# Optimization experiments

Hardware: AMD Instinct MI355X
Metric: run time of the kernel (lower is better)

Reference implementation:

```python
import jax, jax.numpy as jnp
import numpy as np

B, IH, IW = 16, 32, 32
N = IH * IW
HEADS, DIM_HEAD = 8, 64
INNER = HEADS * DIM_HEAD  # 512
INP, OUP = 512, 512
SCALE = DIM_HEAD ** -0.5


def _relative_index():
    # replicate torch.meshgrid (ij) -> coords [2, N]
    yy, xx = np.meshgrid(np.arange(IH), np.arange(IW), indexing='ij')
    coords = np.stack([yy.reshape(-1), xx.reshape(-1)])  # [2, N]
    rel = coords[:, :, None] - coords[:, None, :]        # [2, N, N]
    rel[0] += IH - 1
    rel[1] += IW - 1
    rel[0] *= 2 * IW - 1
    return jnp.asarray(rel.sum(0).reshape(-1), dtype=jnp.int32)  # [N*N]


def setup_inputs() -> dict:
    key = jax.random.key(0)
    k1, k2, k3, k4, k5 = jax.random.split(key, 5)
    x = jax.random.normal(k1, (B, N, INP), dtype=jnp.float32)
    W_qkv = jax.random.normal(k2, (INP, 3 * INNER), dtype=jnp.float32) * (INP ** -0.5)
    # table is initialized to zeros in the module; use small randn so bias path is exercised
    rel_table = jax.random.normal(k3, ((2 * IH - 1) * (2 * IW - 1), HEADS), dtype=jnp.float32) * 0.02
    W_out = jax.random.normal(k4, (INNER, OUP), dtype=jnp.float32) * (INNER ** -0.5)
    b_out = jax.random.normal(k5, (OUP,), dtype=jnp.float32) * 0.02
    return {
        'x': x,
        'W_qkv': W_qkv,
        'rel_table': rel_table,
        'W_out': W_out,
        'b_out': b_out,
        'rel_index': _relative_index(),
    }


def reference(x, W_qkv, rel_table, W_out, b_out, rel_index):
    b, n, _ = x.shape
    qkv = x @ W_qkv                                            # [b, n, 3*inner]
    q, k, v = jnp.split(qkv, 3, axis=-1)
    def to_heads(t):
        return t.reshape(b, n, HEADS, DIM_HEAD).transpose(0, 2, 1, 3)  # [b, h, n, d]
    q, k, v = to_heads(q), to_heads(k), to_heads(v)
    dots = jnp.einsum('bhnd,bhmd->bhnm', q, k) * SCALE         # [b, h, n, n]
    bias = rel_table[rel_index].reshape(n, n, HEADS).transpose(2, 0, 1)[None]  # [1, h, n, n]
    attn = jax.nn.softmax(dots + bias, axis=-1)
    out = jnp.einsum('bhnm,bhmd->bhnd', attn, v)               # [b, h, n, d]
    out = out.transpose(0, 2, 1, 3).reshape(b, n, INNER)       # [b, n, inner]
    return out @ W_out + b_out
```

## Files before the change

### kernel.cpp

```cpp
#include <hip/hip_runtime.h>
#include <math.h>

#define BATCH 16
#define NTOK 1024
#define HEADS 8
#define DHEAD 64
#define INNER 512
#define QKV_COLS 1536
#define SCALE_L2E 0.1803368801111244f
#define LOG2E 1.4426950408889634f

#if __has_builtin(__builtin_amdgcn_exp2f)
#define EXP2F(x) __builtin_amdgcn_exp2f(x)
#else
#define EXP2F(x) __expf((x) * 0.6931471805599453f)
#endif

typedef _Float16 f16x8 __attribute__((ext_vector_type(8)));
typedef _Float16 f16x4 __attribute__((ext_vector_type(4)));
typedef float f32x4 __attribute__((ext_vector_type(4)));

#define MFMA32(a, b, c) __builtin_amdgcn_mfma_f32_16x16x32_f16(a, b, c, 0, 0, 0)

__device__ __forceinline__ void glds16(const void* g, void* l) {
    __builtin_amdgcn_global_load_lds(
        (const __attribute__((address_space(1))) unsigned int*)g,
        (__attribute__((address_space(3))) unsigned int*)l, 16, 0, 0);
}

#define XV (BATCH * NTOK * INNER / 4)
#define WQ (INNER * QKV_COLS)
#define WO (INNER * INNER)

__global__ __launch_bounds__(256)
void convert_inputs(const float* __restrict__ x, const float* __restrict__ Wq,
                    const float* __restrict__ Wo, _Float16* __restrict__ x_h,
                    _Float16* __restrict__ Wq_t, _Float16* __restrict__ Wo_t) {
    int idx = blockIdx.x * 256 + threadIdx.x;
    if (idx < XV) {
        float4 v = ((const float4*)x)[idx];
        f16x4 h;
        h[0] = (_Float16)v.x; h[1] = (_Float16)v.y;
        h[2] = (_Float16)v.z; h[3] = (_Float16)v.w;
        *(f16x4*)(x_h + (size_t)idx * 4) = h;
    } else if (idx < XV + WQ) {
        int i = idx - XV;
        int n = i >> 9, k = i & 511;
        Wq_t[i] = (_Float16)Wq[k * QKV_COLS + n];
    } else if (idx < XV + WQ + WO) {
        int i = idx - XV - WQ;
        int n = i >> 9, k = i & 511;
        Wo_t[i] = (_Float16)Wo[k * INNER + n];
    }
}

template<bool OUT_F16, bool ADD_BIAS>
__global__ __launch_bounds__(256)
void gemm_f16(const _Float16* __restrict__ A, const _Float16* __restrict__ Bt,
              const float* __restrict__ bias, void* __restrict__ Cout,
              int M, int N, int K) {
    __shared__ _Float16 As[128 * 32];
    __shared__ _Float16 Bs[128 * 32];

    const int t    = threadIdx.x;
    const int l    = t & 63;
    const int w    = t >> 6;
    const int wm   = w >> 1;
    const int wn   = w & 1;
    const int quad = l >> 4;
    const int lrow = l & 15;
    const size_t row0 = (size_t)blockIdx.y * 128;
    const size_t col0 = (size_t)blockIdx.x * 128;

    const int srow = t >> 2;
    const int sch  = t & 3;

    f32x4 acc[4][4] = {};

    for (int k0 = 0; k0 < K; k0 += 32) {
        __syncthreads();
        glds16(A + (row0 + srow) * K + k0 + sch * 8,            (char*)As + t * 16);
        glds16(A + (row0 + 64 + srow) * K + k0 + sch * 8,       (char*)As + 4096 + t * 16);
        glds16(Bt + (col0 + srow) * K + k0 + sch * 8,           (char*)Bs + t * 16);
        glds16(Bt + (col0 + 64 + srow) * K + k0 + sch * 8,      (char*)Bs + 4096 + t * 16);
        __syncthreads();

        f16x8 af[4], bf[4];
#pragma unroll
        for (int i = 0; i < 4; ++i)
            af[i] = *(const f16x8*)(As + (wm * 64 + i * 16 + lrow) * 32 + quad * 8);
#pragma unroll
        for (int j = 0; j < 4; ++j)
            bf[j] = *(const f16x8*)(Bs + (wn * 64 + j * 16 + lrow) * 32 + quad * 8);
#pragma unroll
        for (int i = 0; i < 4; ++i)
#pragma unroll
            for (int j = 0; j < 4; ++j)
                acc[i][j] = __builtin_amdgcn_mfma_f32_16x16x32_f16(af[i], bf[j], acc[i][j], 0, 0, 0);
    }

#pragma unroll
    for (int i = 0; i < 4; ++i) {
#pragma unroll
        for (int j = 0; j < 4; ++j) {
            size_t r = row0 + wm * 64 + i * 16 + quad * 4;
            size_t c = col0 + wn * 64 + j * 16 + lrow;
#pragma unroll
            for (int reg = 0; reg < 4; ++reg) {
                float v = acc[i][j][reg];
                if (OUT_F16) {
                    ((_Float16*)Cout)[(r + reg) * N + c] = (_Float16)v;
                } else {
                    if (ADD_BIAS) v += bias[c];
                    ((float*)Cout)[(r + reg) * N + c] = v;
                }
            }
        }
    }
}

__global__ __launch_bounds__(256)
void transpose_v(const _Float16* __restrict__ qkv, _Float16* __restrict__ vt) {
    __shared__ _Float16 T[64][72];
    const int t  = threadIdx.x;
    const int j0 = blockIdx.x * 64;
    const int h  = blockIdx.y, bb = blockIdx.z;
    const int jr = t >> 2;
    const int dc = (t & 3) * 16;
    const _Float16* src = qkv + ((size_t)bb * NTOK + j0 + jr) * QKV_COLS + 2 * INNER + h * DHEAD + dc;
    f16x8 v0 = *(const f16x8*)src;
    f16x8 v1 = *(const f16x8*)(src + 8);
#pragma unroll
    for (int e = 0; e < 8; ++e) { T[jr][dc + e] = v0[e]; T[jr][dc + 8 + e] = v1[e]; }
    __syncthreads();
    const int dr = t >> 2;
    const int jc = (t & 3) * 16;
    f16x8 o0, o1;
#pragma unroll
    for (int e = 0; e < 8; ++e) { o0[e] = T[jc + e][dr]; o1[e] = T[jc + 8 + e][dr]; }
    _Float16* dst = vt + (((size_t)bb * HEADS + h) * 64 + dr) * NTOK + j0 + jc;
    *(f16x8*)dst = o0;
    *(f16x8*)(dst + 8) = o1;
}

__global__ __launch_bounds__(512, 4)
void attn_f16_v6(const _Float16* __restrict__ qkv, const _Float16* __restrict__ vt,
                 const float* __restrict__ rel_table, _Float16* __restrict__ out) {
    __shared__ _Float16 Ks[2][64 * 64];
    __shared__ _Float16 Vs[2][64 * 64];
    __shared__ float biasS[3969];

    const int t    = threadIdx.x;
    const int l    = t & 63;
    const int w    = t >> 6;
    const int quad = l >> 4;
    const int lrow = l & 15;
    const int h    = blockIdx.y;
    const int bb   = blockIdx.z;
    const int qr0  = blockIdx.x * 256 + w * 32;

    for (int idx = t; idx < 3969; idx += 512)
        biasS[idx] = rel_table[idx * HEADS + h] * LOG2E;

    const size_t tokbase = (size_t)bb * NTOK;

    f16x8 aq[2][2];
#pragma unroll
    for (int mt = 0; mt < 2; ++mt)
#pragma unroll
        for (int ksi = 0; ksi < 2; ++ksi)
            aq[mt][ksi] = *(const f16x8*)(qkv + (tokbase + qr0 + mt * 16 + lrow) * QKV_COLS
                                          + h * DHEAD + ksi * 32 + quad * 8);

    f32x4 O[2][4] = {};
    float l0 = 0.f, l1 = 0.f;

    const int iy = qr0 >> 5;
    const int krow_base = 8 * (lrow >> 2) + (lrow & 3);
    const int fKl = (lrow & 3) + 4 * ((lrow >> 2) & 1);

    const int kr  = t >> 3;
    const int ksl = t & 7;
    const int fKr = (kr & 3) + 4 * ((kr >> 3) & 1);
    const _Float16* kbase = qkv + tokbase * QKV_COLS + INNER + h * DHEAD;
    const _Float16* vbase = vt + ((size_t)(bb * HEADS + h) * 64) * NTOK;

    auto stage = [&](int jt, int bufi) {
        const int j0s = jt * 64;
        glds16(kbase + (size_t)(j0s + kr) * QKV_COLS + (ksl ^ fKr) * 8, (char*)Ks[bufi] + t * 16);
        glds16(vbase + (size_t)kr * NTOK + j0s + (ksl ^ (kr & 7)) * 8,  (char*)Vs[bufi] + t * 16);
    };

    stage(0, 0);

    for (int jt = 0; jt < 16; ++jt) {
        const int buf = jt & 1;
        __syncthreads();
        if (jt < 15) stage(jt + 1, buf ^ 1);

#pragma unroll
        for (int jn0 = 0; jn0 < 2; ++jn0) {
            f16x8 pb0, pb1;
#pragma unroll
            for (int s = 0; s < 2; ++s) {
                const int krow = jn0 * 32 + krow_base + 4 * s;
                f32x4 S0 = {}, S1 = {};
#pragma unroll
                for (int ksi = 0; ksi < 2; ++ksi) {
                    f16x8 bk = *(const f16x8*)(Ks[buf] + krow * 64
                                               + (((ksi * 4 + quad) ^ fKl) * 8));
                    S0 = MFMA32(bk, aq[0][ksi], S0);
                    S1 = MFMA32(bk, aq[1][ksi], S1);
                }
                const int base = (iy - (jt * 2 + jn0) + 31) * 63 + 31 + lrow
                                 - 8 * quad - 4 * s;
                {
                    float p0 = EXP2F(fmaf(S0[0], SCALE_L2E, biasS[base - 0]));
                    float p1 = EXP2F(fmaf(S0[1], SCALE_L2E, biasS[base - 1]));
                    float p2 = EXP2F(fmaf(S0[2], SCALE_L2E, biasS[base - 2]));
                    float p3 = EXP2F(fmaf(S0[3], SCALE_L2E, biasS[base - 3]));
                    l0 += (p0 + p1) + (p2 + p3);
                    pb0[s * 4 + 0] = (_Float16)p0; pb0[s * 4 + 1] = (_Float16)p1;
                    pb0[s * 4 + 2] = (_Float16)p2; pb0[s * 4 + 3] = (_Float16)p3;
                }
                {
                    const int b1 = base + 16;
                    float p0 = EXP2F(fmaf(S1[0], SCALE_L2E, biasS[b1 - 0]));
                    float p1 = EXP2F(fmaf(S1[1], SCALE_L2E, biasS[b1 - 1]));
                    float p2 = EXP2F(fmaf(S1[2], SCALE_L2E, biasS[b1 - 2]));
                    float p3 = EXP2F(fmaf(S1[3], SCALE_L2E, biasS[b1 - 3]));
                    l1 += (p0 + p1) + (p2 + p3);
                    pb1[s * 4 + 0] = (_Float16)p0; pb1[s * 4 + 1] = (_Float16)p1;
                    pb1[s * 4 + 2] = (_Float16)p2; pb1[s * 4 + 3] = (_Float16)p3;
                }
            }

#pragma unroll
            for (int dn = 0; dn < 4; ++dn) {
                const int d = dn * 16 + lrow;
                f16x8 av = *(const f16x8*)(Vs[buf] + d * 64
                              + (((jn0 * 4 + quad) ^ (d & 7)) * 8));
                O[0][dn] = MFMA32(av, pb0, O[0][dn]);
                O[1][dn] = MFMA32(av, pb1, O[1][dn]);
            }
        }
    }

#pragma unroll
    for (int mt = 0; mt < 2; ++mt) {
        float s = mt ? l1 : l0;
        s += __shfl_xor(s, 16);
        s += __shfl_xor(s, 32);
        const float inv = 1.f / s;
        const size_t orow = (tokbase + qr0 + mt * 16 + lrow) * INNER + h * DHEAD;
#pragma unroll
        for (int dn = 0; dn < 4; ++dn) {
            const f32x4 o = O[mt][dn];
            f16x4 ov;
            ov[0] = (_Float16)(o[0] * inv); ov[1] = (_Float16)(o[1] * inv);
            ov[2] = (_Float16)(o[2] * inv); ov[3] = (_Float16)(o[3] * inv);
            *(f16x4*)(out + orow + dn * 16 + quad * 4) = ov;
        }
    }
}

extern "C" void kernel_launch(void* const* d_in, const int* in_sizes, int n_in,
                              void* d_out, int out_size, void* d_ws, size_t ws_size,
                              hipStream_t stream) {
    const float* x         = (const float*)d_in[0];
    const float* W_qkv     = (const float*)d_in[1];
    const float* rel_table = (const float*)d_in[2];
    const float* W_out     = (const float*)d_in[3];
    const float* b_out     = (const float*)d_in[4];

    _Float16* x_h   = (_Float16*)d_ws;
    _Float16* Wq_t  = x_h + (size_t)BATCH * NTOK * INNER;
    _Float16* Wo_t  = Wq_t + (size_t)INNER * QKV_COLS;
    _Float16* qkv_h = Wo_t + (size_t)INNER * INNER;
    _Float16* att_h = qkv_h + (size_t)BATCH * NTOK * QKV_COLS;
    _Float16* vt_g  = att_h + (size_t)BATCH * NTOK * INNER;

    const int M = BATCH * NTOK;

    convert_inputs<<<(XV + WQ + WO + 255) / 256, 256, 0, stream>>>(
        x, W_qkv, W_out, x_h, Wq_t, Wo_t);

    gemm_f16<true, false><<<dim3(QKV_COLS / 128, M / 128), 256, 0, stream>>>(
        x_h, Wq_t, nullptr, qkv_h, M, QKV_COLS, INNER);

    transpose_v<<<dim3(NTOK / 64, HEADS, BATCH), 256, 0, stream>>>(qkv_h, vt_g);

    attn_f16_v6<<<dim3(NTOK / 256, HEADS, BATCH), 512, 0, stream>>>(
        qkv_h, vt_g, rel_table, att_h);

    gemm_f16<false, true><<<dim3(INNER / 128, M / 128), 256, 0, stream>>>(
        att_h, Wo_t, b_out, d_out, M, INNER, INNER);
}
```

Baseline: 214.2 us.

## Fuse V transpose into QKV GEMM epilogue and widen GEMM K-tile with swizzle

The QKV GEMM now writes the V columns directly into the transposed per-head layout, which removes the separate transpose_v kernel and its extra pass over V. The GEMM k-tile grows from 32 to 64 and uses an XOR-swizzled shared-memory layout to avoid bank conflicts. MFMA operands are swapped so each lane holds four consecutive columns, which allows vectorized f16x4/float4 epilogue stores. The V-path stores become strided scalar writes along NTOK, and the larger shared tiles raise LDS use per block.

```diff
diff --git a/kernel.cpp b/kernel.cpp
--- a/kernel.cpp
+++ b/kernel.cpp
@@ -54,13 +54,13 @@
     }
 }
 
-template<bool OUT_F16, bool ADD_BIAS>
-__global__ __launch_bounds__(256)
+template<int MODE>
+__global__ __launch_bounds__(256, 4)
 void gemm_f16(const _Float16* __restrict__ A, const _Float16* __restrict__ Bt,
               const float* __restrict__ bias, void* __restrict__ Cout,
-              int M, int N, int K) {
-    __shared__ _Float16 As[128 * 32];
-    __shared__ _Float16 Bs[128 * 32];
+              _Float16* __restrict__ vtg, int M, int N, int K) {
+    __shared__ _Float16 As[128 * 64];
+    __shared__ _Float16 Bs[128 * 64];
 
     const int t    = threadIdx.x;
     const int l    = t & 63;
@@ -72,75 +72,71 @@
     const size_t row0 = (size_t)blockIdx.y * 128;
     const size_t col0 = (size_t)blockIdx.x * 128;
 
-    const int srow = t >> 2;
-    const int sch  = t & 3;
+    const int srow = t >> 3;
+    const int sch  = t & 7;
 
     f32x4 acc[4][4] = {};
 
-    for (int k0 = 0; k0 < K; k0 += 32) {
+    for (int k0 = 0; k0 < K; k0 += 64) {
         __syncthreads();
-        glds16(A + (row0 + srow) * K + k0 + sch * 8,            (char*)As + t * 16);
-        glds16(A + (row0 + 64 + srow) * K + k0 + sch * 8,       (char*)As + 4096 + t * 16);
-        glds16(Bt + (col0 + srow) * K + k0 + sch * 8,           (char*)Bs + t * 16);
-        glds16(Bt + (col0 + 64 + srow) * K + k0 + sch * 8,      (char*)Bs + 4096 + t * 16);
+#pragma unroll
+        for (int p = 0; p < 4; ++p) {
+            const int r  = p * 32 + srow;
+            const int gc = (sch ^ (r & 7)) * 8;
+            glds16(A  + (row0 + r) * K + k0 + gc, (char*)As + p * 4096 + t * 16);
+            glds16(Bt + (col0 + r) * K + k0 + gc, (char*)Bs + p * 4096 + t * 16);
+        }
         __syncthreads();
 
-        f16x8 af[4], bf[4];
-#pragma unroll
-        for (int i = 0; i < 4; ++i)
-            af[i] = *(const f16x8*)(As + (wm * 64 + i * 16 + lrow) * 32 + quad * 8);
-#pragma unroll
-        for (int j = 0; j < 4; ++j)
-            bf[j] = *(const f16x8*)(Bs + (wn * 64 + j * 16 + lrow) * 32 + quad * 8);
-#pragma unroll
-        for (int i = 0; i < 4; ++i)
-#pragma unroll
-            for (int j = 0; j < 4; ++j)
-                acc[i][j] = __builtin_amdgcn_mfma_f32_16x16x32_f16(af[i], bf[j], acc[i][j], 0, 0, 0);
-    }
-
+#pragma unroll
+        for (int ks = 0; ks < 2; ++ks) {
+            f16x8 af[4], bf[4];
+#pragma unroll
+            for (int i = 0; i < 4; ++i) {
+                const int r = wm * 64 + i * 16 + lrow;
+                af[i] = *(const f16x8*)(As + r * 64 + (((ks * 4 + quad) ^ (r & 7)) * 8));
+            }
+#pragma unroll
+            for (int j = 0; j < 4; ++j) {
+                const int r = wn * 64 + j * 16 + lrow;
+                bf[j] = *(const f16x8*)(Bs + r * 64 + (((ks * 4 + quad) ^ (r & 7)) * 8));
+            }
+#pragma unroll
+            for (int i = 0; i < 4; ++i)
+#pragma unroll
+                for (int j = 0; j < 4; ++j)
+                    acc[i][j] = MFMA32(bf[j], af[i], acc[i][j]);
+        }
+    }
+
+    const bool isV = (MODE == 2) && (col0 >= 2 * INNER);
 #pragma unroll
     for (int i = 0; i < 4; ++i) {
+        const size_t m = row0 + wm * 64 + i * 16 + lrow;
 #pragma unroll
         for (int j = 0; j < 4; ++j) {
-            size_t r = row0 + wm * 64 + i * 16 + quad * 4;
-            size_t c = col0 + wn * 64 + j * 16 + lrow;
-#pragma unroll
-            for (int reg = 0; reg < 4; ++reg) {
-                float v = acc[i][j][reg];
-                if (OUT_F16) {
-                    ((_Float16*)Cout)[(r + reg) * N + c] = (_Float16)v;
-                } else {
-                    if (ADD_BIAS) v += bias[c];
-                    ((float*)Cout)[(r + reg) * N + c] = v;
-                }
-            }
-        }
-    }
-}
-
-__global__ __launch_bounds__(256)
-void transpose_v(const _Float16* __restrict__ qkv, _Float16* __restrict__ vt) {
-    __shared__ _Float16 T[64][72];
-    const int t  = threadIdx.x;
-    const int j0 = blockIdx.x * 64;
-    const int h  = blockIdx.y, bb = blockIdx.z;
-    const int jr = t >> 2;
-    const int dc = (t & 3) * 16;
-    const _Float16* src = qkv + ((size_t)bb * NTOK + j0 + jr) * QKV_COLS + 2 * INNER + h * DHEAD + dc;
-    f16x8 v0 = *(const f16x8*)src;
-    f16x8 v1 = *(const f16x8*)(src + 8);
-#pragma unroll
-    for (int e = 0; e < 8; ++e) { T[jr][dc + e] = v0[e]; T[jr][dc + 8 + e] = v1[e]; }
-    __syncthreads();
-    const int dr = t >> 2;
-    const int jc = (t & 3) * 16;
-    f16x8 o0, o1;
-#pragma unroll
-    for (int e = 0; e < 8; ++e) { o0[e] = T[jc + e][dr]; o1[e] = T[jc + 8 + e][dr]; }
-    _Float16* dst = vt + (((size_t)bb * HEADS + h) * 64 + dr) * NTOK + j0 + jc;
-    *(f16x8*)dst = o0;
-    *(f16x8*)(dst + 8) = o1;
+            const size_t c = col0 + wn * 64 + j * 16 + quad * 4;
+            f32x4 v = acc[i][j];
+            if (MODE == 0) {
+                float4 bv = *(const float4*)(bias + c);
+                v[0] += bv.x; v[1] += bv.y; v[2] += bv.z; v[3] += bv.w;
+                *(f32x4*)((float*)Cout + m * N + c) = v;
+            } else if (!isV) {
+                f16x4 hv;
+                hv[0] = (_Float16)v[0]; hv[1] = (_Float16)v[1];
+                hv[2] = (_Float16)v[2]; hv[3] = (_Float16)v[3];
+                *(f16x4*)((_Float16*)Cout + m * N + c) = hv;
+            } else {
+                const int cv = (int)(c - 2 * INNER);
+                const int hh = cv >> 6, db = cv & 63;
+                const size_t vb = (((size_t)(m >> 10) * HEADS + hh) * 64 + db) * NTOK
+                                  + (m & (NTOK - 1));
+#pragma unroll
+                for (int reg = 0; reg < 4; ++reg)
+                    vtg[vb + (size_t)reg * NTOK] = (_Float16)v[reg];
+            }
+        }
+    }
 }
 
 __global__ __launch_bounds__(512, 4)
@@ -285,14 +281,12 @@
     convert_inputs<<<(XV + WQ + WO + 255) / 256, 256, 0, stream>>>(
         x, W_qkv, W_out, x_h, Wq_t, Wo_t);
 
-    gemm_f16<true, false><<<dim3(QKV_COLS / 128, M / 128), 256, 0, stream>>>(
-        x_h, Wq_t, nullptr, qkv_h, M, QKV_COLS, INNER);
-
-    transpose_v<<<dim3(NTOK / 64, HEADS, BATCH), 256, 0, stream>>>(qkv_h, vt_g);
+    gemm_f16<2><<<dim3(QKV_COLS / 128, M / 128), 256, 0, stream>>>(
+        x_h, Wq_t, nullptr, qkv_h, vt_g, M, QKV_COLS, INNER);
 
     attn_f16_v6<<<dim3(NTOK / 256, HEADS, BATCH), 512, 0, stream>>>(
         qkv_h, vt_g, rel_table, att_h);
 
-    gemm_f16<false, true><<<dim3(INNER / 128, M / 128), 256, 0, stream>>>(
-        att_h, Wo_t, b_out, d_out, M, INNER, INNER);
-}
+    gemm_f16<0><<<dim3(INNER / 128, M / 128), 256, 0, stream>>>(
+        att_h, Wo_t, b_out, d_out, nullptr, M, INNER, INNER);
+}
```

New measurement: 214.2 us. No clear change (+0.0%).
